# Performance work log

Hardware: AMD Instinct MI355X
Metric: run time of the kernel (lower is better)

## Reference

```python
import jax, jax.numpy as jnp
import numpy as np

B, SD, AD, M, MAXC = 65536, 32, 1, 32, 2  # batch, state_dim, action_dim, msg_dim, max_children


def _l2norm(x):
    # F.normalize(x, dim=-1) with eps=1e-12
    return x / jnp.maximum(jnp.linalg.norm(x, axis=-1, keepdims=True), 1e-12)


def _mlp(x, w1, b1, w2, b2, w3, b3):
    # MLPBase: Linear->ReLU->Linear->ReLU->Linear (400/300 hidden)
    h = jax.nn.relu(x @ w1 + b1)
    h = jax.nn.relu(h @ w2 + b2)
    return h @ w3 + b3


def setup_inputs() -> dict:
    key = jax.random.key(0)
    ks = iter(jax.random.split(key, 40))

    def p(shape):
        return jax.random.normal(next(ks), shape, jnp.float32) * 0.05

    inp = {
        "state": jax.random.normal(next(ks), (B, SD), jnp.float32),
        "action": jax.random.normal(next(ks), (B, AD), jnp.float32),
        # CriticUp params
        "up_fc1_w": p((SD + AD, 64)), "up_fc1_b": p((64,)),
        "up_fc2_w": p((64 + M, 64)), "up_fc2_b": p((64,)),
        "up_fc3_w": p((64, M)), "up_fc3_b": p((M,)),
        "att_w": p((9 + SD, M)), "att_b": p((M,)),
    }
    q_in = 12 + M + AD + M   # rel_pos(12) + self_input(msg_dim) + action + msg_down
    m_in = 12 + M + M        # rel_pos(12) + self_input + msg_down
    for n, d, out in (("q1", q_in, 1), ("q2", q_in, 1), ("msg", m_in, M * MAXC)):
        inp[n + "_w1"] = p((d, 400)); inp[n + "_b1"] = p((400,))
        inp[n + "_w2"] = p((400, 300)); inp[n + "_b2"] = p((300,))
        inp[n + "_w3"] = p((300, out)); inp[n + "_b3"] = p((out,))
    return inp


def reference(state, action,
              up_fc1_w, up_fc1_b, up_fc2_w, up_fc2_b, up_fc3_w, up_fc3_b,
              att_w, att_b,
              q1_w1, q1_b1, q1_w2, q1_b2, q1_w3, q1_b3,
              q2_w1, q2_b1, q2_w2, q2_b2, q2_w3, q2_b3,
              msg_w1, msg_b1, msg_w2, msg_b2, msg_w3, msg_b3):
    b = state.shape[0]
    # ---- bottom-up (num_limbs=1: root has no children -> zero child states/messages) ----
    xu = _l2norm(jnp.concatenate([state, action], -1) @ up_fc1_w + up_fc1_b)  # [b,64]
    ch_states = jnp.zeros((b, MAXC, 9 + SD), state.dtype)
    att = jax.nn.softmax(ch_states @ att_w + att_b, axis=-2)                  # [b,MAXC,M]
    m_up = (jnp.zeros((b, MAXC, M), state.dtype) * att).sum(-2)              # [b,M] (zeros)
    h = jnp.tanh(jnp.concatenate([xu, m_up], -1))
    h = jnp.tanh(h @ up_fc2_w + up_fc2_b)
    msg_up = _l2norm(h @ up_fc3_w + up_fc3_b)                                 # [b,M]
    # ---- top-down (root's parent index -1 wraps to itself -> zero relative offsets) ----
    pos = state[:, :3]
    rel = jnp.concatenate([jnp.zeros((b, 6), state.dtype), pos, pos], -1)     # [b,12]
    m_td = jnp.zeros((b, M), state.dtype)                                     # sliced from zero parent_msg
    xum = jnp.concatenate([rel, msg_up, action, m_td], -1)
    x1 = _mlp(xum, q1_w1, q1_b1, q1_w2, q1_b2, q1_w3, q1_b3)                  # [b,1]
    x2 = _mlp(xum, q2_w1, q2_b1, q2_w2, q2_b2, q2_w3, q2_b3)                  # [b,1]
    xm = jnp.tanh(jnp.concatenate([rel, msg_up, m_td], -1))
    msg_down = _l2norm(_mlp(xm, msg_w1, msg_b1, msg_w2, msg_b2, msg_w3, msg_b3))
    del msg_down  # computed per torch forward but unused in single-limb output
    # stack over 1 limb then sum over limb dim == identity
    return (x1, x2)
```

## Files before the change

kernel.cpp:

```cpp
#include <hip/hip_runtime.h>
#include <math.h>


#define BTOT   65536
#define XUM_OFF 655360ull

#define PK_BLK  78
#define PH_THR  512
#define PH_ROWS 256
#define PH_BLK  (BTOT / PH_ROWS)
#define F1W 0
#define F1B 2112
#define F2W 2176
#define F2B 6272
#define F3W 6336
#define F3B 8384
#define W0_FLOATS 8416

#define ML_THR  512
#define ML_ROWS 128
#define ML_BLK  (BTOT / ML_ROWS)
#define H1S     428

typedef float  f32x4 __attribute__((ext_vector_type(4)));
typedef __bf16 bf16x8 __attribute__((ext_vector_type(8)));
typedef unsigned short u16x8 __attribute__((ext_vector_type(8)));
typedef unsigned short u16x4 __attribute__((ext_vector_type(4)));
typedef unsigned int   u32x2 __attribute__((ext_vector_type(2)));

__device__ __forceinline__ unsigned short f2b(float f) {
  union { float f; unsigned int u; } v; v.f = f;
  return (unsigned short)((v.u + 0x7fffu + ((v.u >> 16) & 1u)) >> 16);
}
__device__ __forceinline__ float b2f(unsigned short u) {
  union { unsigned int u; float f; } v; v.u = ((unsigned int)u) << 16;
  return v.f;
}
__device__ __forceinline__ f32x4 MFMA(bf16x8 a, bf16x8 b, f32x4 c) {
  return __builtin_amdgcn_mfma_f32_16x16x32_bf16(a, b, c, 0, 0, 0);
}
__device__ __forceinline__ bf16x8 ld8(const unsigned short* p) {
  return __builtin_bit_cast(bf16x8, *(const u16x8*)p);
}
__device__ __forceinline__ float ftanh(float x) {
  float e = __builtin_amdgcn_exp2f(x * 2.885390081777927f);
  return (e - 1.0f) * __builtin_amdgcn_rcpf(e + 1.0f);
}

struct P0 {
  const float* state; const float* action;
  const float* f1w; const float* f1b;
  const float* f2w; const float* f2b;
  const float* f3w; const float* f3b;
  const float* q1w1; const float* q1b1; const float* q1w2;
  const float* q2w1; const float* q2b1; const float* q2w2;
  unsigned short* ws;
  unsigned short* xum;
};

__global__ __launch_bounds__(PH_THR, 2) void phase0_kernel(P0 P) {
  __shared__ float w0[W0_FLOATS];
  __shared__ unsigned short hx[PH_ROWS * 68];
  const int tid = threadIdx.x;

  if (blockIdx.x < PK_BLK) {
    const int gid = blockIdx.x * PH_THR + tid;
    const int lane = gid & 63, f = gid >> 6;
    const int q = f / 312, fl = f - q * 312;
    const float* w1 = q ? P.q2w1 : P.q1w1;
    const float* b1 = q ? P.q2b1 : P.q1b1;
    const float* w2 = q ? P.q2w2 : P.q1w2;
    int nt, ks; const bool isw1 = (fl < 52);
    if (isw1) { nt = fl >> 1; ks = fl & 1; }
    else      { int fl2 = fl - 52; nt = fl2 / 13; ks = fl2 - nt * 13; }
    const int col = nt * 16 + (lane & 15);
    const int k0  = ks * 32 + (lane >> 4) * 8;
    unsigned short v[8];
    #pragma unroll
    for (int j = 0; j < 8; ++j) {
      const int k = k0 + j;
      float x = 0.f;
      if (isw1) {
        if (col < 400) {
          if (k < 39) x = w1[(6 + k) * 400 + col];
          else if (k == 39) x = b1[col];
        }
      } else {
        if (k < 400 && col < 300) x = w2[k * 300 + col];
      }
      v[j] = f2b(x);
    }
    *(u16x8*)(P.ws + (size_t)f * 512 + lane * 8) = *(const u16x8*)v;
    return;
  }

  const int rid = tid >> 2, sub = tid & 3, j0 = sub * 16;
  const long g0 = (long)(blockIdx.x - PK_BLK) * PH_ROWS + rid;
  const long g1 = g0 + 128;

  for (int i = tid; i < 528;  i += PH_THR) *(f32x4*)(w0 + F1W + 4*i) = *(const f32x4*)(P.f1w + 4*i);
  for (int i = tid; i < 16;   i += PH_THR) *(f32x4*)(w0 + F1B + 4*i) = *(const f32x4*)(P.f1b + 4*i);
  for (int i = tid; i < 1024; i += PH_THR) *(f32x4*)(w0 + F2W + 4*i) = *(const f32x4*)(P.f2w + 4*i);
  for (int i = tid; i < 16;   i += PH_THR) *(f32x4*)(w0 + F2B + 4*i) = *(const f32x4*)(P.f2b + 4*i);
  for (int i = tid; i < 512;  i += PH_THR) *(f32x4*)(w0 + F3W + 4*i) = *(const f32x4*)(P.f3w + 4*i);
  for (int i = tid; i < 8;    i += PH_THR) *(f32x4*)(w0 + F3B + 4*i) = *(const f32x4*)(P.f3b + 4*i);

  {
    float sa0[33], sa1[33];
    {
      const float4* sp0 = (const float4*)(P.state + g0 * 32);
      const float4* sp1 = (const float4*)(P.state + g1 * 32);
      #pragma unroll
      for (int c = 0; c < 8; ++c) {
        float4 a = sp0[c], b = sp1[c];
        sa0[c*4+0] = a.x; sa0[c*4+1] = a.y; sa0[c*4+2] = a.z; sa0[c*4+3] = a.w;
        sa1[c*4+0] = b.x; sa1[c*4+1] = b.y; sa1[c*4+2] = b.z; sa1[c*4+3] = b.w;
      }
      sa0[32] = P.action[g0];
      sa1[32] = P.action[g1];
    }
    __syncthreads();
    float a0[16], a1[16];
    #pragma unroll
    for (int j = 0; j < 16; ++j) { a0[j] = w0[F1B + j0 + j]; a1[j] = a0[j]; }
    #pragma unroll 4
    for (int i = 0; i < 33; ++i) {
      const float s0 = sa0[i], s1 = sa1[i];
      const f32x4* wr = (const f32x4*)&w0[F1W + i * 64 + j0];
      #pragma unroll
      for (int c = 0; c < 4; ++c) {
        f32x4 wv = wr[c];
        #pragma unroll
        for (int u = 0; u < 4; ++u) {
          a0[c*4+u] += s0 * wv[u];
          a1[c*4+u] += s1 * wv[u];
        }
      }
    }
    float ss0 = 0.f, ss1 = 0.f;
    #pragma unroll
    for (int j = 0; j < 16; ++j) { ss0 += a0[j] * a0[j]; ss1 += a1[j] * a1[j]; }
    ss0 += __shfl_xor(ss0, 1, 64); ss0 += __shfl_xor(ss0, 2, 64);
    ss1 += __shfl_xor(ss1, 1, 64); ss1 += __shfl_xor(ss1, 2, 64);
    const float sc0 = 1.f / fmaxf(sqrtf(ss0), 1e-12f);
    const float sc1 = 1.f / fmaxf(sqrtf(ss1), 1e-12f);
    #pragma unroll
    for (int j = 0; j < 16; ++j) {
      hx[rid * 68 + j0 + j]        = f2b(ftanh(a0[j] * sc0));
      hx[(rid + 128) * 68 + j0 + j] = f2b(ftanh(a1[j] * sc1));
    }
  }
  __syncthreads();
  {
    float a0[16], a1[16];
    #pragma unroll
    for (int j = 0; j < 16; ++j) { a0[j] = w0[F2B + j0 + j]; a1[j] = a0[j]; }
    #pragma unroll 2
    for (int i0 = 0; i0 < 16; ++i0) {
      const u16x4 h0 = *(const u16x4*)&hx[rid * 68 + i0 * 4];
      const u16x4 h1v = *(const u16x4*)&hx[(rid + 128) * 68 + i0 * 4];
      #pragma unroll
      for (int u = 0; u < 4; ++u) {
        const float v0 = b2f(h0[u]), v1 = b2f(h1v[u]);
        const f32x4* wr = (const f32x4*)&w0[F2W + (i0 * 4 + u) * 64 + j0];
        #pragma unroll
        for (int c = 0; c < 4; ++c) {
          f32x4 wv = wr[c];
          #pragma unroll
          for (int t = 0; t < 4; ++t) {
            a0[c*4+t] += v0 * wv[t];
            a1[c*4+t] += v1 * wv[t];
          }
        }
      }
    }
    __syncthreads();
    #pragma unroll
    for (int j = 0; j < 16; ++j) {
      hx[rid * 68 + j0 + j]        = f2b(ftanh(a0[j]));
      hx[(rid + 128) * 68 + j0 + j] = f2b(ftanh(a1[j]));
    }
  }
  __syncthreads();
  const int j0m = sub * 8;
  float m0[8], m1[8];
  #pragma unroll
  for (int j = 0; j < 8; ++j) { m0[j] = w0[F3B + j0m + j]; m1[j] = m0[j]; }
  #pragma unroll 2
  for (int i0 = 0; i0 < 16; ++i0) {
    const u16x4 h0 = *(const u16x4*)&hx[rid * 68 + i0 * 4];
    const u16x4 h1v = *(const u16x4*)&hx[(rid + 128) * 68 + i0 * 4];
    #pragma unroll
    for (int u = 0; u < 4; ++u) {
      const float v0 = b2f(h0[u]), v1 = b2f(h1v[u]);
      const f32x4* wr = (const f32x4*)&w0[F3W + (i0 * 4 + u) * 32 + j0m];
      #pragma unroll
      for (int c = 0; c < 2; ++c) {
        f32x4 wv = wr[c];
        #pragma unroll
        for (int t = 0; t < 4; ++t) {
          m0[c*4+t] += v0 * wv[t];
          m1[c*4+t] += v1 * wv[t];
        }
      }
    }
  }
  float sm0 = 0.f, sm1 = 0.f;
  #pragma unroll
  for (int j = 0; j < 8; ++j) { sm0 += m0[j] * m0[j]; sm1 += m1[j] * m1[j]; }
  sm0 += __shfl_xor(sm0, 1, 64); sm0 += __shfl_xor(sm0, 2, 64);
  sm1 += __shfl_xor(sm1, 1, 64); sm1 += __shfl_xor(sm1, 2, 64);
  const float sc0 = 1.f / fmaxf(sqrtf(sm0), 1e-12f);
  const float sc1 = 1.f / fmaxf(sqrtf(sm1), 1e-12f);
  __syncthreads();
  #pragma unroll
  for (int j = 0; j < 8; ++j) {
    hx[rid * 68 + j0m + j]        = f2b(m0[j] * sc0);
    hx[(rid + 128) * 68 + j0m + j] = f2b(m1[j] * sc1);
  }
  __syncthreads();
  #pragma unroll
  for (int rr = 0; rr < 2; ++rr) {
    const long gr = rr ? g1 : g0;
    const int  lr = rid + rr * 128;
    float pos[3];
    pos[0] = P.state[gr * 32 + 0];
    pos[1] = P.state[gr * 32 + 1];
    pos[2] = P.state[gr * 32 + 2];
    const float act = P.action[gr];
    u16x8 v0, v1;
    #pragma unroll
    for (int t = 0; t < 16; ++t) {
      const int c = j0 + t;
      unsigned short u;
      if      (c < 3)  u = f2b(pos[c]);
      else if (c < 6)  u = f2b(pos[c - 3]);
      else if (c < 38) u = hx[lr * 68 + (c - 6)];
      else if (c == 38) u = f2b(act);
      else if (c == 39) u = 0x3f80;
      else              u = 0;
      if (t < 8) v0[t] = u; else v1[t - 8] = u;
    }
    unsigned short* dst = P.xum + (size_t)gr * 64 + j0;
    *(u16x8*)dst = v0;
    *(u16x8*)(dst + 8) = v1;
  }
}

struct P1 {
  const unsigned short* img; const unsigned short* xum;
  const float* q1b2; const float* q1w3; const float* q1b3;
  const float* q2b2; const float* q2w3; const float* q2b3;
  float* out;
};

__global__ __launch_bounds__(ML_THR, 2) void mlp_kernel(P1 P) {
  __shared__ __align__(16) unsigned short h1[ML_ROWS * H1S];
  __shared__ float xred[ML_ROWS * 4];

  const int tid  = threadIdx.x;
  const int lane = tid & 63, w = tid >> 6;
  const int rl = lane & 15, g = lane >> 4;

  const int rp = w & 3, ch = w >> 2;
  const int wm = w >> 2, wn = w & 3;

  const unsigned short* xr0 = P.xum + ((size_t)blockIdx.x * ML_ROWS + rp * 32 + rl) * 64;
  const bf16x8 af0k0 = ld8(xr0 + g * 8);
  const bf16x8 af0k1 = ld8(xr0 + 32 + g * 8);
  const unsigned short* xr1 = xr0 + 16 * 64;
  const bf16x8 af1k0 = ld8(xr1 + g * 8);
  const bf16x8 af1k1 = ld8(xr1 + 32 + g * 8);

  for (int q = 0; q < 2; ++q) {
    {
      const unsigned short* w1f = P.img + ((size_t)(q * 312 + ch * 26)) * 512 + lane * 8;
      unsigned short* h1w0 = &h1[(size_t)(rp * 32 + rl) * H1S + ch * 208 + g * 4];
      unsigned short* h1w1 = &h1[(size_t)(rp * 32 + 16 + rl) * H1S + ch * 208 + g * 4];
      bf16x8 wA0 = ld8(w1f + 0 * 512), wA1 = ld8(w1f + 1 * 512);
      bf16x8 wB0 = ld8(w1f + 2 * 512), wB1 = ld8(w1f + 3 * 512);
      for (int t = 0; t < 13; t += 2) {
        {
          f32x4 a = (f32x4){0.f, 0.f, 0.f, 0.f};
          f32x4 b = (f32x4){0.f, 0.f, 0.f, 0.f};
          a = MFMA(wA0, af0k0, a); a = MFMA(wA1, af0k1, a);
          b = MFMA(wA0, af1k0, b); b = MFMA(wA1, af1k1, b);
          if (t + 2 < 13) {
            wA0 = ld8(w1f + (size_t)((t + 2) * 2) * 512);
            wA1 = ld8(w1f + (size_t)((t + 2) * 2 + 1) * 512);
          }
          unsigned int p01, p23, q01, q23;
          const float a0 = fmaxf(a[0], 0.f), a1 = fmaxf(a[1], 0.f);
          const float a2 = fmaxf(a[2], 0.f), a3 = fmaxf(a[3], 0.f);
          const float b0 = fmaxf(b[0], 0.f), b1 = fmaxf(b[1], 0.f);
          const float b2 = fmaxf(b[2], 0.f), b3 = fmaxf(b[3], 0.f);
          asm("v_cvt_pk_bf16_f32 %0, %1, %2" : "=v"(p01) : "v"(a0), "v"(a1));
          asm("v_cvt_pk_bf16_f32 %0, %1, %2" : "=v"(p23) : "v"(a2), "v"(a3));
          asm("v_cvt_pk_bf16_f32 %0, %1, %2" : "=v"(q01) : "v"(b0), "v"(b1));
          asm("v_cvt_pk_bf16_f32 %0, %1, %2" : "=v"(q23) : "v"(b2), "v"(b3));
          u32x2 pk; pk[0] = p01; pk[1] = p23;
          u32x2 qk; qk[0] = q01; qk[1] = q23;
          *(u32x2*)(h1w0 + t * 16) = pk;
          *(u32x2*)(h1w1 + t * 16) = qk;
        }
        if (t + 1 < 13) {
          f32x4 a = (f32x4){0.f, 0.f, 0.f, 0.f};
          f32x4 b = (f32x4){0.f, 0.f, 0.f, 0.f};
          a = MFMA(wB0, af0k0, a); a = MFMA(wB1, af0k1, a);
          b = MFMA(wB0, af1k0, b); b = MFMA(wB1, af1k1, b);
          if (t + 3 < 13) {
            wB0 = ld8(w1f + (size_t)((t + 3) * 2) * 512);
            wB1 = ld8(w1f + (size_t)((t + 3) * 2 + 1) * 512);
          }
          unsigned int p01, p23, q01, q23;
          const float a0 = fmaxf(a[0], 0.f), a1 = fmaxf(a[1], 0.f);
          const float a2 = fmaxf(a[2], 0.f), a3 = fmaxf(a[3], 0.f);
          const float b0 = fmaxf(b[0], 0.f), b1 = fmaxf(b[1], 0.f);
          const float b2 = fmaxf(b[2], 0.f), b3 = fmaxf(b[3], 0.f);
          asm("v_cvt_pk_bf16_f32 %0, %1, %2" : "=v"(p01) : "v"(a0), "v"(a1));
          asm("v_cvt_pk_bf16_f32 %0, %1, %2" : "=v"(p23) : "v"(a2), "v"(a3));
          asm("v_cvt_pk_bf16_f32 %0, %1, %2" : "=v"(q01) : "v"(b0), "v"(b1));
          asm("v_cvt_pk_bf16_f32 %0, %1, %2" : "=v"(q23) : "v"(b2), "v"(b3));
          u32x2 pk; pk[0] = p01; pk[1] = p23;
          u32x2 qk; qk[0] = q01; qk[1] = q23;
          *(u32x2*)(h1w0 + (t + 1) * 16) = pk;
          *(u32x2*)(h1w1 + (t + 1) * 16) = qk;
        }
      }
    }
    __syncthreads();

    f32x4 acc2[4][5];
    #pragma unroll
    for (int mt = 0; mt < 4; ++mt)
      #pragma unroll
      for (int jn = 0; jn < 5; ++jn) acc2[mt][jn] = (f32x4){0.f, 0.f, 0.f, 0.f};
    {
      const unsigned short* w2f = P.img + ((size_t)(q * 312 + 52 + wn * 65)) * 512 + lane * 8;
      bf16x8 bA[5], bB[5];
      #pragma unroll
      for (int jn = 0; jn < 5; ++jn) bA[jn] = ld8(w2f + (size_t)(jn * 13 + 0) * 512);
      #pragma unroll
      for (int jn = 0; jn < 5; ++jn) bB[jn] = ld8(w2f + (size_t)(jn * 13 + 1) * 512);
      for (int ks = 0; ks < 13; ks += 2) {
        {
          bf16x8 am[4];
          #pragma unroll
          for (int mt = 0; mt < 4; ++mt)
            am[mt] = ld8(&h1[(size_t)(wm * 64 + mt * 16 + rl) * H1S + ks * 32 + g * 8]);
          #pragma unroll
          for (int jn = 0; jn < 5; ++jn)
            #pragma unroll
            for (int mt = 0; mt < 4; ++mt)
              acc2[mt][jn] = MFMA(am[mt], bA[jn], acc2[mt][jn]);
          if (ks + 2 < 13) {
            #pragma unroll
            for (int jn = 0; jn < 5; ++jn)
              bA[jn] = ld8(w2f + (size_t)(jn * 13 + ks + 2) * 512);
          }
        }
        if (ks + 1 < 13) {
          bf16x8 am[4];
          #pragma unroll
          for (int mt = 0; mt < 4; ++mt)
            am[mt] = ld8(&h1[(size_t)(wm * 64 + mt * 16 + rl) * H1S + (ks + 1) * 32 + g * 8]);
          #pragma unroll
          for (int jn = 0; jn < 5; ++jn)
            #pragma unroll
            for (int mt = 0; mt < 4; ++mt)
              acc2[mt][jn] = MFMA(am[mt], bB[jn], acc2[mt][jn]);
          if (ks + 3 < 13) {
            #pragma unroll
            for (int jn = 0; jn < 5; ++jn)
              bB[jn] = ld8(w2f + (size_t)(jn * 13 + ks + 3) * 512);
          }
        }
      }
    }

    const float* b2p = q ? P.q2b2 : P.q1b2;
    const float* w3  = q ? P.q2w3 : P.q1w3;
    const float* b3  = q ? P.q2b3 : P.q1b3;
    float xp[4][4];
    #pragma unroll
    for (int mt = 0; mt < 4; ++mt)
      #pragma unroll
      for (int i = 0; i < 4; ++i) xp[mt][i] = 0.f;
    #pragma unroll
    for (int jn = 0; jn < 5; ++jn) {
      const int n = wn * 80 + jn * 16 + rl;
      if (n < 300) {
        const float bv = b2p[n], wv = w3[n];
        #pragma unroll
        for (int mt = 0; mt < 4; ++mt)
          #pragma unroll
          for (int i = 0; i < 4; ++i)
            xp[mt][i] += fmaxf(acc2[mt][jn][i] + bv, 0.f) * wv;
      }
    }
    #pragma unroll
    for (int off = 1; off < 16; off <<= 1)
      #pragma unroll
      for (int mt = 0; mt < 4; ++mt)
        #pragma unroll
        for (int i = 0; i < 4; ++i)
          xp[mt][i] += __shfl_xor(xp[mt][i], off, 64);
    if (rl == 0) {
      #pragma unroll
      for (int mt = 0; mt < 4; ++mt)
        #pragma unroll
        for (int i = 0; i < 4; ++i)
          xred[(wm * 64 + mt * 16 + g * 4 + i) * 4 + wn] = xp[mt][i];
    }
    __syncthreads();
    if (tid < ML_ROWS) {
      const float4 xv = *(const float4*)&xred[tid * 4];
      P.out[(size_t)q * BTOT + (size_t)blockIdx.x * ML_ROWS + tid] =
          xv.x + xv.y + xv.z + xv.w + b3[0];
    }
    __syncthreads();
  }
}

extern "C" void kernel_launch(void* const* d_in, const int* in_sizes, int n_in,
                              void* d_out, int out_size, void* d_ws, size_t ws_size,
                              hipStream_t stream) {
  (void)in_sizes; (void)n_in; (void)out_size; (void)ws_size;
  P0 A;
  A.state  = (const float*)d_in[0];
  A.action = (const float*)d_in[1];
  A.f1w = (const float*)d_in[2]; A.f1b = (const float*)d_in[3];
  A.f2w = (const float*)d_in[4]; A.f2b = (const float*)d_in[5];
  A.f3w = (const float*)d_in[6]; A.f3b = (const float*)d_in[7];
  A.q1w1 = (const float*)d_in[10]; A.q1b1 = (const float*)d_in[11]; A.q1w2 = (const float*)d_in[12];
  A.q2w1 = (const float*)d_in[16]; A.q2b1 = (const float*)d_in[17]; A.q2w2 = (const float*)d_in[18];
  A.ws  = (unsigned short*)d_ws;
  A.xum = (unsigned short*)((unsigned char*)d_ws + XUM_OFF);
  phase0_kernel<<<dim3(PK_BLK + PH_BLK), dim3(PH_THR), 0, stream>>>(A);

  P1 B;
  B.img  = (const unsigned short*)d_ws;
  B.xum  = (const unsigned short*)((unsigned char*)d_ws + XUM_OFF);
  B.q1b2 = (const float*)d_in[13]; B.q1w3 = (const float*)d_in[14]; B.q1b3 = (const float*)d_in[15];
  B.q2b2 = (const float*)d_in[19]; B.q2w3 = (const float*)d_in[20]; B.q2b3 = (const float*)d_in[21];
  B.out  = (float*)d_out;
  mlp_kernel<<<dim3(ML_BLK), dim3(ML_THR), 0, stream>>>(B);
}
```

Baseline: 105.1 us.

## Double MLP block rows and split layer-1 into K halves feeding layer 2

```diff
diff --git a/kernel.cpp b/kernel.cpp
--- a/kernel.cpp
+++ b/kernel.cpp
@@ -17,10 +17,10 @@
 #define F3B 8384
 #define W0_FLOATS 8416
 
-#define ML_THR  512
-#define ML_ROWS 128
+#define ML_THR  1024
+#define ML_ROWS 256
 #define ML_BLK  (BTOT / ML_ROWS)
-#define H1S     428
+#define H1S     228
 
 typedef float  f32x4 __attribute__((ext_vector_type(4)));
 typedef __bf16 bf16x8 __attribute__((ext_vector_type(8)));
@@ -146,7 +146,7 @@
     const float sc1 = 1.f / fmaxf(sqrtf(ss1), 1e-12f);
     #pragma unroll
     for (int j = 0; j < 16; ++j) {
-      hx[rid * 68 + j0 + j]        = f2b(ftanh(a0[j] * sc0));
+      hx[rid * 68 + j0 + j]         = f2b(ftanh(a0[j] * sc0));
       hx[(rid + 128) * 68 + j0 + j] = f2b(ftanh(a1[j] * sc1));
     }
   }
@@ -177,7 +177,7 @@
     __syncthreads();
     #pragma unroll
     for (int j = 0; j < 16; ++j) {
-      hx[rid * 68 + j0 + j]        = f2b(ftanh(a0[j]));
+      hx[rid * 68 + j0 + j]         = f2b(ftanh(a0[j]));
       hx[(rid + 128) * 68 + j0 + j] = f2b(ftanh(a1[j]));
     }
   }
@@ -215,7 +215,7 @@
   __syncthreads();
   #pragma unroll
   for (int j = 0; j < 8; ++j) {
-    hx[rid * 68 + j0m + j]        = f2b(m0[j] * sc0);
+    hx[rid * 68 + j0m + j]         = f2b(m0[j] * sc0);
     hx[(rid + 128) * 68 + j0m + j] = f2b(m1[j] * sc1);
   }
   __syncthreads();
@@ -254,7 +254,7 @@
   float* out;
 };
 
-__global__ __launch_bounds__(ML_THR, 2) void mlp_kernel(P1 P) {
+__global__ __launch_bounds__(ML_THR) void mlp_kernel(P1 P) {
   __shared__ __align__(16) unsigned short h1[ML_ROWS * H1S];
   __shared__ float xred[ML_ROWS * 4];
 
@@ -262,7 +262,7 @@
   const int lane = tid & 63, w = tid >> 6;
   const int rl = lane & 15, g = lane >> 4;
 
-  const int rp = w & 3, ch = w >> 2;
+  const int rp = w & 7, ch = w >> 3;
   const int wm = w >> 2, wn = w & 3;
 
   const unsigned short* xr0 = P.xum + ((size_t)blockIdx.x * ML_ROWS + rp * 32 + rl) * 64;
@@ -273,109 +273,64 @@
   const bf16x8 af1k1 = ld8(xr1 + 32 + g * 8);
 
   for (int q = 0; q < 2; ++q) {
-    {
-      const unsigned short* w1f = P.img + ((size_t)(q * 312 + ch * 26)) * 512 + lane * 8;
-      unsigned short* h1w0 = &h1[(size_t)(rp * 32 + rl) * H1S + ch * 208 + g * 4];
-      unsigned short* h1w1 = &h1[(size_t)(rp * 32 + 16 + rl) * H1S + ch * 208 + g * 4];
-      bf16x8 wA0 = ld8(w1f + 0 * 512), wA1 = ld8(w1f + 1 * 512);
-      bf16x8 wB0 = ld8(w1f + 2 * 512), wB1 = ld8(w1f + 3 * 512);
-      for (int t = 0; t < 13; t += 2) {
-        {
-          f32x4 a = (f32x4){0.f, 0.f, 0.f, 0.f};
-          f32x4 b = (f32x4){0.f, 0.f, 0.f, 0.f};
-          a = MFMA(wA0, af0k0, a); a = MFMA(wA1, af0k1, a);
-          b = MFMA(wA0, af1k0, b); b = MFMA(wA1, af1k1, b);
-          if (t + 2 < 13) {
-            wA0 = ld8(w1f + (size_t)((t + 2) * 2) * 512);
-            wA1 = ld8(w1f + (size_t)((t + 2) * 2 + 1) * 512);
-          }
-          unsigned int p01, p23, q01, q23;
-          const float a0 = fmaxf(a[0], 0.f), a1 = fmaxf(a[1], 0.f);
-          const float a2 = fmaxf(a[2], 0.f), a3 = fmaxf(a[3], 0.f);
-          const float b0 = fmaxf(b[0], 0.f), b1 = fmaxf(b[1], 0.f);
-          const float b2 = fmaxf(b[2], 0.f), b3 = fmaxf(b[3], 0.f);
-          asm("v_cvt_pk_bf16_f32 %0, %1, %2" : "=v"(p01) : "v"(a0), "v"(a1));
-          asm("v_cvt_pk_bf16_f32 %0, %1, %2" : "=v"(p23) : "v"(a2), "v"(a3));
-          asm("v_cvt_pk_bf16_f32 %0, %1, %2" : "=v"(q01) : "v"(b0), "v"(b1));
-          asm("v_cvt_pk_bf16_f32 %0, %1, %2" : "=v"(q23) : "v"(b2), "v"(b3));
-          u32x2 pk; pk[0] = p01; pk[1] = p23;
-          u32x2 qk; qk[0] = q01; qk[1] = q23;
-          *(u32x2*)(h1w0 + t * 16) = pk;
-          *(u32x2*)(h1w1 + t * 16) = qk;
-        }
-        if (t + 1 < 13) {
-          f32x4 a = (f32x4){0.f, 0.f, 0.f, 0.f};
-          f32x4 b = (f32x4){0.f, 0.f, 0.f, 0.f};
-          a = MFMA(wB0, af0k0, a); a = MFMA(wB1, af0k1, a);
-          b = MFMA(wB0, af1k0, b); b = MFMA(wB1, af1k1, b);
-          if (t + 3 < 13) {
-            wB0 = ld8(w1f + (size_t)((t + 3) * 2) * 512);
-            wB1 = ld8(w1f + (size_t)((t + 3) * 2 + 1) * 512);
-          }
-          unsigned int p01, p23, q01, q23;
-          const float a0 = fmaxf(a[0], 0.f), a1 = fmaxf(a[1], 0.f);
-          const float a2 = fmaxf(a[2], 0.f), a3 = fmaxf(a[3], 0.f);
-          const float b0 = fmaxf(b[0], 0.f), b1 = fmaxf(b[1], 0.f);
-          const float b2 = fmaxf(b[2], 0.f), b3 = fmaxf(b[3], 0.f);
-          asm("v_cvt_pk_bf16_f32 %0, %1, %2" : "=v"(p01) : "v"(a0), "v"(a1));
-          asm("v_cvt_pk_bf16_f32 %0, %1, %2" : "=v"(p23) : "v"(a2), "v"(a3));
-          asm("v_cvt_pk_bf16_f32 %0, %1, %2" : "=v"(q01) : "v"(b0), "v"(b1));
-          asm("v_cvt_pk_bf16_f32 %0, %1, %2" : "=v"(q23) : "v"(b2), "v"(b3));
-          u32x2 pk; pk[0] = p01; pk[1] = p23;
-          u32x2 qk; qk[0] = q01; qk[1] = q23;
-          *(u32x2*)(h1w0 + (t + 1) * 16) = pk;
-          *(u32x2*)(h1w1 + (t + 1) * 16) = qk;
-        }
-      }
-    }
-    __syncthreads();
-
     f32x4 acc2[4][5];
     #pragma unroll
     for (int mt = 0; mt < 4; ++mt)
       #pragma unroll
       for (int jn = 0; jn < 5; ++jn) acc2[mt][jn] = (f32x4){0.f, 0.f, 0.f, 0.f};
-    {
-      const unsigned short* w2f = P.img + ((size_t)(q * 312 + 52 + wn * 65)) * 512 + lane * 8;
-      bf16x8 bA[5], bB[5];
-      #pragma unroll
-      for (int jn = 0; jn < 5; ++jn) bA[jn] = ld8(w2f + (size_t)(jn * 13 + 0) * 512);
-      #pragma unroll
-      for (int jn = 0; jn < 5; ++jn) bB[jn] = ld8(w2f + (size_t)(jn * 13 + 1) * 512);
-      for (int ks = 0; ks < 13; ks += 2) {
-        {
+
+    #pragma unroll
+    for (int kh = 0; kh < 2; ++kh) {
+      const int NTO  = kh ? 14 : 0;
+      const int HALF = kh ? 6 : 7;
+      const int KSO  = kh ? 7 : 0;
+      const int KSk  = kh ? 6 : 7;
+
+      for (int t = 0; t < HALF; ++t) {
+        const int cnt = ch * HALF + t;
+        const int nt  = NTO + cnt;
+        const unsigned short* wf = P.img + ((size_t)(q * 312 + nt * 2)) * 512 + lane * 8;
+        const bf16x8 b0 = ld8(wf);
+        const bf16x8 b1 = ld8(wf + 512);
+        f32x4 a = (f32x4){0.f, 0.f, 0.f, 0.f};
+        f32x4 b = (f32x4){0.f, 0.f, 0.f, 0.f};
+        a = MFMA(b0, af0k0, a); a = MFMA(b1, af0k1, a);
+        b = MFMA(b0, af1k0, b); b = MFMA(b1, af1k1, b);
+        const float a0 = fmaxf(a[0], 0.f), a1 = fmaxf(a[1], 0.f);
+        const float a2 = fmaxf(a[2], 0.f), a3 = fmaxf(a[3], 0.f);
+        const float c0 = fmaxf(b[0], 0.f), c1 = fmaxf(b[1], 0.f);
+        const float c2 = fmaxf(b[2], 0.f), c3 = fmaxf(b[3], 0.f);
+        unsigned int p01, p23, q01, q23;
+        asm("v_cvt_pk_bf16_f32 %0, %1, %2" : "=v"(p01) : "v"(a0), "v"(a1));
+        asm("v_cvt_pk_bf16_f32 %0, %1, %2" : "=v"(p23) : "v"(a2), "v"(a3));
+        asm("v_cvt_pk_bf16_f32 %0, %1, %2" : "=v"(q01) : "v"(c0), "v"(c1));
+        asm("v_cvt_pk_bf16_f32 %0, %1, %2" : "=v"(q23) : "v"(c2), "v"(c3));
+        u32x2 pk; pk[0] = p01; pk[1] = p23;
+        u32x2 qk; qk[0] = q01; qk[1] = q23;
+        *(u32x2*)&h1[(size_t)(rp * 32 + rl) * H1S + cnt * 16 + g * 4]      = pk;
+        *(u32x2*)&h1[(size_t)(rp * 32 + 16 + rl) * H1S + cnt * 16 + g * 4] = qk;
+      }
+      __syncthreads();
+
+      {
+        const unsigned short* w2f =
+            P.img + ((size_t)(q * 312 + 52 + wn * 65)) * 512 + lane * 8;
+        for (int ks = 0; ks < KSk; ++ks) {
+          const int ksg = KSO + ks;
           bf16x8 am[4];
           #pragma unroll
           for (int mt = 0; mt < 4; ++mt)
             am[mt] = ld8(&h1[(size_t)(wm * 64 + mt * 16 + rl) * H1S + ks * 32 + g * 8]);
           #pragma unroll
-          for (int jn = 0; jn < 5; ++jn)
+          for (int jn = 0; jn < 5; ++jn) {
+            const bf16x8 bf = ld8(w2f + (size_t)(jn * 13 + ksg) * 512);
             #pragma unroll
             for (int mt = 0; mt < 4; ++mt)
-              acc2[mt][jn] = MFMA(am[mt], bA[jn], acc2[mt][jn]);
-          if (ks + 2 < 13) {
-            #pragma unroll
-            for (int jn = 0; jn < 5; ++jn)
-              bA[jn] = ld8(w2f + (size_t)(jn * 13 + ks + 2) * 512);
+              acc2[mt][jn] = MFMA(am[mt], bf, acc2[mt][jn]);
           }
         }
-        if (ks + 1 < 13) {
-          bf16x8 am[4];
-          #pragma unroll
-          for (int mt = 0; mt < 4; ++mt)
-            am[mt] = ld8(&h1[(size_t)(wm * 64 + mt * 16 + rl) * H1S + (ks + 1) * 32 + g * 8]);
-          #pragma unroll
-          for (int jn = 0; jn < 5; ++jn)
-            #pragma unroll
-            for (int mt = 0; mt < 4; ++mt)
-              acc2[mt][jn] = MFMA(am[mt], bB[jn], acc2[mt][jn]);
-          if (ks + 3 < 13) {
-            #pragma unroll
-            for (int jn = 0; jn < 5; ++jn)
-              bB[jn] = ld8(w2f + (size_t)(jn * 13 + ks + 3) * 512);
-          }
-        }
-      }
+      }
+      __syncthreads();
     }
 
     const float* b2p = q ? P.q2b2 : P.q1b2;
```

Measured after the change: 155.9 us. 1.48x slower.
